# Kernel optimization log

Hardware: AMD Instinct MI355X
Metric: run time of the kernel (lower is better)

## Reference

```python
import jax, jax.numpy as jnp
from jax import lax
import numpy as np

NUM_HEADS = 8
KW = 3  # window kernel size

def _avgpool3(x):
    # x: [B,C,H,W]; AvgPool2d(3,1,1) with count_include_pad=True -> sum/9
    s = lax.reduce_window(x, 0.0, lax.add, (1, 1, KW, KW), (1, 1, 1, 1),
                          ((0, 0), (0, 0), (1, 1), (1, 1)))
    return s / (KW * KW)

def _unfold3(y):
    # y: [B,h,w,C] -> [B,h,w,9,C]; patch index ordered row-major (kh,kw)
    B, h, w, C = y.shape
    yp = jnp.pad(y, ((0, 0), (1, 1), (1, 1), (0, 0)))
    return jnp.stack([yp[:, i:i + h, j:j + w, :]
                      for i in range(KW) for j in range(KW)], axis=3)

def setup_inputs():
    key = jax.random.key(0)
    ks = jax.random.split(key, 9)
    B, C, H, W = 8, 256, 64, 64
    sd = 0.02
    return {
        "x": jax.random.normal(ks[0], (B, C, H, W), jnp.float32),
        "W_qkv": jax.random.normal(ks[1], (4 * C, C), jnp.float32) * sd,
        "b_qkv": jnp.zeros((4 * C,), jnp.float32),
        "W1": jax.random.normal(ks[2], (C // 2, C), jnp.float32) * sd,
        "b1": jnp.zeros((C // 2,), jnp.float32),
        "W2": jax.random.normal(ks[3], (C, C // 2), jnp.float32) * sd,
        "b2": jnp.zeros((C,), jnp.float32),
        "Wp": jax.random.normal(ks[4], (C, C), jnp.float32) * sd,
        "bp": jnp.zeros((C,), jnp.float32),
    }

def reference(x, W_qkv, b_qkv, W1, b1, W2, b2, Wp, bp):
    B, C, H, W = x.shape
    nH = NUM_HEADS
    hd = C // nH
    scale = hd ** -0.5
    # avg pool (stride 1 keeps spatial dims), to channels-last
    y = _avgpool3(x).transpose(0, 2, 3, 1)                 # [B,h,w,C]
    qkv = y @ W_qkv.T + b_qkv                              # [B,h,w,4C]
    qkv = qkv.reshape(B, H, W, C, 4)
    q, k, v, chans = qkv[..., 0], qkv[..., 1], qkv[..., 2], qkv[..., 3]
    # channel gate
    g = jax.nn.sigmoid(jax.nn.relu(chans @ W1.T + b1) @ W2.T + b2)  # [B,h,w,C]
    # local window attention: each query attends to its 3x3 neighborhood
    qh = q.reshape(B, H, W, nH, hd)                        # [B,h,w,n,d]
    kp = _unfold3(k).reshape(B, H, W, KW * KW, nH, hd)     # [B,h,w,9,n,d]
    vp = _unfold3(v).reshape(B, H, W, KW * KW, nH, hd)
    attn = jnp.einsum('bhwnd,bhwknd->bhwnk', qh, kp) * scale
    attn = jax.nn.softmax(attn, axis=-1)
    out = jnp.einsum('bhwnk,bhwknd->bhwnd', attn, vp).reshape(B, H, W, C)
    out = out * g + out
    out = out @ Wp.T + bp
    return out.transpose(0, 3, 1, 2)                       # [B,C,H,W]
```

## Files before the change

### kernel.cpp

```cpp
#include <hip/hip_runtime.h>
#include <stdint.h>

typedef __bf16    bf16x8 __attribute__((ext_vector_type(8)));
typedef float     f32x4  __attribute__((ext_vector_type(4)));
typedef uint32_t  u32x4  __attribute__((ext_vector_type(4)));
typedef uint32_t  u32x2  __attribute__((ext_vector_type(2)));

#define MFMA(a,b,c) __builtin_amdgcn_mfma_f32_16x16x32_bf16((a),(b),(c),0,0,0)

__device__ __align__(16) uint16_t g_y [8*64*64*256];
__device__ __align__(16) uint16_t g_wpk[393216];

#define WQF 0
#define WKF 65536
#define WVF 131072
#define WCF 196608
#define W1F 262144
#define W2F 294912
#define WPF 327680

static __device__ __forceinline__ float b2f(uint32_t u){ return __builtin_bit_cast(float, u<<16); }
static __device__ __forceinline__ float blo(uint32_t u){ return __builtin_bit_cast(float, u<<16); }
static __device__ __forceinline__ float bhi(uint32_t u){ return __builtin_bit_cast(float, u & 0xffff0000u); }
static __device__ __forceinline__ uint16_t f2bn(float f){
  return __builtin_bit_cast(uint16_t, (__bf16)f);
}
static __device__ __forceinline__ uint32_t pk2(float x, float y){
  return (uint32_t)f2bn(x) | ((uint32_t)f2bn(y) << 16);
}

__global__ __launch_bounds__(512) void kprep(const float* __restrict__ x,
    const float* __restrict__ Wqkv, const float* __restrict__ W1,
    const float* __restrict__ W2, const float* __restrict__ Wp){
  int t = threadIdx.x;
  int bid = blockIdx.x;
  if (bid < 1024){
    __shared__ __align__(16) uint16_t sm[3*128*82];
    uint32_t* smw = (uint32_t*)sm;
    int b = bid >> 7, h = (bid >> 1) & 63, ch = (bid & 1) << 7;
    for (int i=t; i<384; i+=512){
      int base = i*41;
      smw[base+3]  = 0;
      smw[base+36] = 0;
    }
    if (h==0 || h==63){
      int hh = (h==0) ? 0 : 2;
      for (int i=t; i<5248; i+=512) smw[hh*5248 + i] = 0;
    }
    #pragma unroll
    for (int i=0;i<12;i++){
      int id = t + 512*i;
      int w4 = id&15, c = (id>>4)&127, hh = id>>11;
      int gy = h - 1 + hh;
      if ((unsigned)gy < 64u){
        f32x4 ld = *(const f32x4*)&x[(((b*256+ch+c)*64+gy)*64) + w4*4];
        int wb = (((hh*128+c)*82 + 8 + w4*4) >> 1);
        smw[wb+0] = pk2(ld[0], ld[1]);
        smw[wb+1] = pk2(ld[2], ld[3]);
      }
    }
    __syncthreads();
    int c = t & 127, wsel = t >> 7;
    int r0 = c*82, r1 = r0 + 128*82, r2 = r1 + 128*82;
    int w0 = wsel*16;
    float csp = b2f(sm[r0+w0+7]) + b2f(sm[r1+w0+7]) + b2f(sm[r2+w0+7]);
    float csc = b2f(sm[r0+w0+8]) + b2f(sm[r1+w0+8]) + b2f(sm[r2+w0+8]);
    uint16_t* dst = g_y + ((b*64+h)*64)*256 + ch + c;
    for (int j2=0;j2<16;j2++){
      int w = w0 + j2;
      float csn = b2f(sm[r0+w+9]) + b2f(sm[r1+w+9]) + b2f(sm[r2+w+9]);
      float yv = (csp + csc + csn) * (1.0f/9.0f);
      dst[w*256] = f2bn(yv);
      csp = csc; csc = csn;
    }
  } else {
    int idx = (bid - 1024)*512 + t;
    int j = idx & 7, lane = (idx>>3)&63;
    int n16 = lane & 15, q4 = lane>>4;
    float v;
    if (idx < 262144){
      int tt = idx >> 16, l = idx & 65535;
      int s = (l>>9)&7, nt = l>>12;
      v = Wqkv[(4*(nt*16+n16) + tt)*256 + s*32 + q4*8 + j];
    } else if (idx < 294912){
      int l = idx - 262144;
      int s = (l>>9)&7, nt = l>>12;
      v = W1[(nt*16+n16)*256 + s*32 + q4*8 + j];
    } else if (idx < 327680){
      int l = idx - 294912;
      int s = (l>>9)&3, nt = l>>11;
      v = W2[(nt*16+n16)*128 + s*32 + q4*8 + j];
    } else {
      int l = idx - 327680;
      int s = (l>>9)&7, nt = l>>12;
      v = Wp[(nt*16+n16)*256 + s*32 + q4*8 + j];
    }
    g_wpk[idx] = f2bn(v);
  }
}

#define YSTR  264
#define QA    15840
#define QB    20192
#define KS    24544
#define VS    32704
#define HSTR  136
#define MCH   0
#define MHS   8448
#define MAO   15840
#define MAOSTR 266
#define MAOT  15840
#define MTSTR 36

static __device__ __forceinline__ void attn_pass(const uint16_t* sm, int qbase,
    int lane, int wave, uint32_t* opk){
  int p = lane & 31, half = lane >> 5;
  int cb = wave*32 + half*16;
  const uint16_t* qp = &sm[qbase + p*HSTR + cb];
  u32x4 qa = *(const u32x4*)qp;
  u32x4 qb = *(const u32x4*)(qp+8);
  float qv[16];
  #pragma unroll
  for (int i=0;i<4;i++){
    qv[2*i]    = blo(qa[i]); qv[2*i+1]   = bhi(qa[i]);
    qv[8+2*i]  = blo(qb[i]); qv[8+2*i+1] = bhi(qb[i]);
  }
  int hb = 10*(p>>3) + (p&7) + 11;
  const int off[9] = {-11,-10,-9,-1,0,1,9,10,11};
  float sc[9];
  #pragma unroll
  for (int nb=0;nb<9;nb++){
    const uint16_t* kp = &sm[KS + (hb+off[nb])*HSTR + cb];
    u32x4 ka = *(const u32x4*)kp;
    u32x4 kb = *(const u32x4*)(kp+8);
    float s = 0.f;
    #pragma unroll
    for (int i=0;i<4;i++){
      s += qv[2*i]*blo(ka[i])   + qv[2*i+1]*bhi(ka[i]);
      s += qv[8+2*i]*blo(kb[i]) + qv[8+2*i+1]*bhi(kb[i]);
    }
    s += __shfl_xor(s, 32);
    sc[nb] = s * 0.17677669529663687f;
  }
  float mx = sc[0];
  #pragma unroll
  for (int nb=1;nb<9;nb++) mx = fmaxf(mx, sc[nb]);
  float l = 0.f;
  #pragma unroll
  for (int nb=0;nb<9;nb++){ sc[nb] = __expf(sc[nb]-mx); l += sc[nb]; }
  float inv = 1.f / l;
  float o[16];
  #pragma unroll
  for (int i=0;i<16;i++) o[i]=0.f;
  #pragma unroll
  for (int nb=0;nb<9;nb++){
    float wgt = sc[nb]*inv;
    const uint16_t* vp = &sm[VS + (hb+off[nb])*HSTR + cb];
    u32x4 va = *(const u32x4*)vp;
    u32x4 vb = *(const u32x4*)(vp+8);
    #pragma unroll
    for (int i=0;i<4;i++){
      o[2*i]    += wgt*blo(va[i]); o[2*i+1]   += wgt*bhi(va[i]);
      o[8+2*i]  += wgt*blo(vb[i]); o[8+2*i+1] += wgt*bhi(vb[i]);
    }
  }
  #pragma unroll
  for (int i=0;i<8;i++) opk[i] = pk2(o[2*i], o[2*i+1]);
}

__global__ __launch_bounds__(512,4) void kattn(const float* __restrict__ bqkv,
    const float* __restrict__ b1, const float* __restrict__ b2v,
    const float* __restrict__ bp, float* __restrict__ out){
  __shared__ __align__(16) uint16_t sm[40864];
  int t = threadIdx.x;
  int lane = t & 63, wave = t >> 6;
  int n16 = lane & 15, quad = lane >> 4;
  int bid = blockIdx.x;
  int bb = bid >> 7, ty = (bid >> 3) & 15, tx = bid & 7;

  uint32_t opk0[8], opk1[8];
  uint32_t chp[8];

  int hrow0 = 10*(n16>>3) + (n16&7) + 11;
  int hrow1 = hrow0 + 20;

  #pragma unroll
  for (int i=0;i<4;i++){
    int id = t + 512*i;
    if (id < 1920){
      int hp = id >> 5, c8 = id & 31;
      int py = hp/10, px = hp - py*10;
      int gy = ty*4 + py - 1, gx = tx*8 + px - 1;
      u32x4 ld = {0,0,0,0};
      if ((unsigned)gy<64u && (unsigned)gx<64u)
        ld = *(const u32x4*)&g_y[((bb*64+gy)*64+gx)*256 + c8*8];
      *(u32x4*)&sm[hp*YSTR + c8*8] = ld;
    }
  }
  __syncthreads();

  {
    int ntgQ = wave, ntC0 = wave*2, ntC1 = wave*2+1;
    f32x4 aq0={0.f,0.f,0.f,0.f}, aq1={0.f,0.f,0.f,0.f};
    f32x4 c00={0.f,0.f,0.f,0.f}, c01={0.f,0.f,0.f,0.f};
    f32x4 c10={0.f,0.f,0.f,0.f}, c11={0.f,0.f,0.f,0.f};
    #pragma unroll
    for (int s=0;s<8;s++){
      bf16x8 Bq  = *(const bf16x8*)&g_wpk[WQF + ((ntgQ*8+s)*64+lane)*8];
      bf16x8 Bc0 = *(const bf16x8*)&g_wpk[WCF + ((ntC0*8+s)*64+lane)*8];
      bf16x8 Bc1 = *(const bf16x8*)&g_wpk[WCF + ((ntC1*8+s)*64+lane)*8];
      bf16x8 A0 = *(const bf16x8*)&sm[hrow0*YSTR + s*32 + quad*8];
      bf16x8 A1 = *(const bf16x8*)&sm[hrow1*YSTR + s*32 + quad*8];
      aq0 = MFMA(A0,Bq,aq0);  aq1 = MFMA(A1,Bq,aq1);
      c00 = MFMA(A0,Bc0,c00); c01 = MFMA(A1,Bc0,c01);
      c10 = MFMA(A0,Bc1,c10); c11 = MFMA(A1,Bc1,c11);
    }
    float bq  = bqkv[4*(ntgQ*16+n16) + 0];
    float bc0 = bqkv[4*(ntC0*16+n16) + 3];
    float bc1 = bqkv[4*(ntC1*16+n16) + 3];
    int colB = wave*16;
    #pragma unroll
    for (int r=0;r<4;r++){
      sm[QA + (quad*4+r)*HSTR + colB + n16]      = f2bn(aq0[r]+bq);
      sm[QA + (16+quad*4+r)*HSTR + colB + n16]   = f2bn(aq1[r]+bq);
    }
    chp[0] = pk2(c00[0]+bc0, c00[1]+bc0); chp[1] = pk2(c00[2]+bc0, c00[3]+bc0);
    chp[2] = pk2(c01[0]+bc0, c01[1]+bc0); chp[3] = pk2(c01[2]+bc0, c01[3]+bc0);
    chp[4] = pk2(c10[0]+bc1, c10[1]+bc1); chp[5] = pk2(c10[2]+bc1, c10[3]+bc1);
    chp[6] = pk2(c11[0]+bc1, c11[1]+bc1); chp[7] = pk2(c11[2]+bc1, c11[3]+bc1);
  }
  {
    int ntg = wave;
    bf16x8 Bk[8], Bv[8];
    #pragma unroll
    for (int s=0;s<8;s++){
      Bk[s] = *(const bf16x8*)&g_wpk[WKF + ((ntg*8+s)*64+lane)*8];
      Bv[s] = *(const bf16x8*)&g_wpk[WVF + ((ntg*8+s)*64+lane)*8];
    }
    float bk = bqkv[4*(ntg*16+n16) + 1];
    float bv = bqkv[4*(ntg*16+n16) + 2];
    int colB = wave*16;
    #pragma unroll
    for (int mt=0; mt<4; mt++){
      f32x4 ak = {0.f,0.f,0.f,0.f}, av = {0.f,0.f,0.f,0.f};
      int m = mt*16 + n16;
      int mr = (m < 60) ? m : 59;
      #pragma unroll
      for (int s=0;s<8;s++){
        bf16x8 A = *(const bf16x8*)&sm[mr*YSTR + s*32 + quad*8];
        ak = MFMA(A, Bk[s], ak);
        av = MFMA(A, Bv[s], av);
      }
      #pragma unroll
      for (int r=0;r<4;r++){
        int row = mt*16 + quad*4 + r;
        if (row < 60){
          int py = row/10, px = row - py*10;
          int gy = ty*4 + py - 1, gx = tx*8 + px - 1;
          bool ok = ((unsigned)gy<64u) && ((unsigned)gx<64u);
          sm[KS + row*HSTR + colB + n16] = ok ? f2bn(ak[r] + bk) : (uint16_t)0;
          sm[VS + row*HSTR + colB + n16] = ok ? f2bn(av[r] + bv) : (uint16_t)0;
        }
      }
    }
  }
  __syncthreads();

  if (wave < 4){
    attn_pass(sm, QA, lane, wave, opk0);
  } else {
    int nt0 = 8 + (wave-4)*2, nt1 = nt0 + 1;
    f32x4 a00={0.f,0.f,0.f,0.f}, a01={0.f,0.f,0.f,0.f};
    f32x4 a10={0.f,0.f,0.f,0.f}, a11={0.f,0.f,0.f,0.f};
    #pragma unroll
    for (int s=0;s<8;s++){
      bf16x8 B0 = *(const bf16x8*)&g_wpk[WQF + ((nt0*8+s)*64+lane)*8];
      bf16x8 B1 = *(const bf16x8*)&g_wpk[WQF + ((nt1*8+s)*64+lane)*8];
      bf16x8 A0 = *(const bf16x8*)&sm[hrow0*YSTR + s*32 + quad*8];
      bf16x8 A1 = *(const bf16x8*)&sm[hrow1*YSTR + s*32 + quad*8];
      a00 = MFMA(A0,B0,a00); a01 = MFMA(A1,B0,a01);
      a10 = MFMA(A0,B1,a10); a11 = MFMA(A1,B1,a11);
    }
    float bq0 = bqkv[4*(nt0*16+n16) + 0];
    float bq1 = bqkv[4*(nt1*16+n16) + 0];
    int c0 = (nt0-8)*16, c1 = (nt1-8)*16;
    #pragma unroll
    for (int r=0;r<4;r++){
      sm[QB + (quad*4+r)*HSTR + c0 + n16]    = f2bn(a00[r]+bq0);
      sm[QB + (16+quad*4+r)*HSTR + c0 + n16] = f2bn(a01[r]+bq0);
      sm[QB + (quad*4+r)*HSTR + c1 + n16]    = f2bn(a10[r]+bq1);
      sm[QB + (16+quad*4+r)*HSTR + c1 + n16] = f2bn(a11[r]+bq1);
    }
  }
  __syncthreads();

  {
    int ntg = 8 + wave;
    bf16x8 Bk[8], Bv[8];
    #pragma unroll
    for (int s=0;s<8;s++){
      Bk[s] = *(const bf16x8*)&g_wpk[WKF + ((ntg*8+s)*64+lane)*8];
      Bv[s] = *(const bf16x8*)&g_wpk[WVF + ((ntg*8+s)*64+lane)*8];
    }
    float bk = bqkv[4*(ntg*16+n16) + 1];
    float bv = bqkv[4*(ntg*16+n16) + 2];
    int colB = wave*16;
    #pragma unroll
    for (int mt=0; mt<4; mt++){
      f32x4 ak = {0.f,0.f,0.f,0.f}, av = {0.f,0.f,0.f,0.f};
      int m = mt*16 + n16;
      int mr = (m < 60) ? m : 59;
      #pragma unroll
      for (int s=0;s<8;s++){
        bf16x8 A = *(const bf16x8*)&sm[mr*YSTR + s*32 + quad*8];
        ak = MFMA(A, Bk[s], ak);
        av = MFMA(A, Bv[s], av);
      }
      #pragma unroll
      for (int r=0;r<4;r++){
        int row = mt*16 + quad*4 + r;
        if (row < 60){
          int py = row/10, px = row - py*10;
          int gy = ty*4 + py - 1, gx = tx*8 + px - 1;
          bool ok = ((unsigned)gy<64u) && ((unsigned)gx<64u);
          sm[KS + row*HSTR + colB + n16] = ok ? f2bn(ak[r] + bk) : (uint16_t)0;
          sm[VS + row*HSTR + colB + n16] = ok ? f2bn(av[r] + bv) : (uint16_t)0;
        }
      }
    }
  }
  __syncthreads();

  #pragma unroll
  for (int jj=0;jj<2;jj++){
    int col = (wave*2+jj)*16 + n16;
    #pragma unroll
    for (int mt=0;mt<2;mt++){
      #pragma unroll
      for (int r2=0;r2<2;r2++){
        uint32_t v = chp[(jj*2+mt)*2+r2];
        int row = mt*16 + quad*4 + r2*2;
        sm[MCH + row*264 + col]     = (uint16_t)(v & 0xffffu);
        sm[MCH + (row+1)*264 + col] = (uint16_t)(v >> 16);
      }
    }
  }
  if (wave < 4) attn_pass(sm, QB, lane, wave, opk1);
  __syncthreads();

  if (wave < 4){
    int p = lane & 31, half = lane >> 5;
    int cb = wave*32 + half*16;
    #pragma unroll
    for (int i=0;i<8;i++){
      *(uint32_t*)&sm[MAO + p*MAOSTR + cb + 2*i]       = opk0[i];
      *(uint32_t*)&sm[MAO + p*MAOSTR + 128 + cb + 2*i] = opk1[i];
    }
  }
  {
    int ntg = wave;
    bf16x8 Bf[8];
    #pragma unroll
    for (int s=0;s<8;s++) Bf[s] = *(const bf16x8*)&g_wpk[W1F + ((ntg*8+s)*64+lane)*8];
    float bs = b1[ntg*16+n16];
    int colB = wave*16;
    #pragma unroll
    for (int mt=0;mt<2;mt++){
      f32x4 a = {0.f,0.f,0.f,0.f};
      #pragma unroll
      for (int s=0;s<8;s++){
        bf16x8 A = *(const bf16x8*)&sm[MCH + (mt*16+n16)*264 + s*32 + quad*8];
        a = MFMA(A, Bf[s], a);
      }
      #pragma unroll
      for (int r=0;r<4;r++){
        int row = mt*16 + quad*4 + r;
        sm[MHS + row*HSTR + colB + n16] = f2bn(fmaxf(a[r]+bs, 0.f));
      }
    }
  }
  __syncthreads();

  {
    int nt0 = wave*2, nt1 = nt0+1;
    f32x4 g00={0.f,0.f,0.f,0.f}, g01={0.f,0.f,0.f,0.f};
    f32x4 g10={0.f,0.f,0.f,0.f}, g11={0.f,0.f,0.f,0.f};
    #pragma unroll
    for (int s=0;s<4;s++){
      bf16x8 B0 = *(const bf16x8*)&g_wpk[W2F + ((nt0*4+s)*64+lane)*8];
      bf16x8 B1 = *(const bf16x8*)&g_wpk[W2F + ((nt1*4+s)*64+lane)*8];
      bf16x8 A0 = *(const bf16x8*)&sm[MHS + n16*HSTR + s*32 + quad*8];
      bf16x8 A1 = *(const bf16x8*)&sm[MHS + (16+n16)*HSTR + s*32 + quad*8];
      g00 = MFMA(A0,B0,g00); g01 = MFMA(A1,B0,g01);
      g10 = MFMA(A0,B1,g10); g11 = MFMA(A1,B1,g11);
    }
    float bs0 = b2v[nt0*16+n16], bs1 = b2v[nt1*16+n16];
    #pragma unroll
    for (int jj=0;jj<2;jj++){
      int colB = (wave*2+jj)*16;
      float bs = jj ? bs1 : bs0;
      #pragma unroll
      for (int mt=0;mt<2;mt++){
        f32x4 a = jj ? (mt ? g11 : g10) : (mt ? g01 : g00);
        #pragma unroll
        for (int r=0;r<4;r++){
          int row = mt*16 + quad*4 + r;
          float gg = 1.f/(1.f+__expf(-(a[r] + bs)));
          float ao = b2f((uint32_t)sm[MAO + row*MAOSTR + colB + n16]);
          sm[MCH + row*264 + colB + n16] = f2bn(ao*(1.f+gg));
        }
      }
    }
  }
  __syncthreads();

  {
    int nt0 = wave*2, nt1 = nt0+1;
    f32x4 p00={0.f,0.f,0.f,0.f}, p01={0.f,0.f,0.f,0.f};
    f32x4 p10={0.f,0.f,0.f,0.f}, p11={0.f,0.f,0.f,0.f};
    #pragma unroll
    for (int s=0;s<8;s++){
      bf16x8 B0 = *(const bf16x8*)&g_wpk[WPF + ((nt0*8+s)*64+lane)*8];
      bf16x8 B1 = *(const bf16x8*)&g_wpk[WPF + ((nt1*8+s)*64+lane)*8];
      bf16x8 A0 = *(const bf16x8*)&sm[MCH + n16*264 + s*32 + quad*8];
      bf16x8 A1 = *(const bf16x8*)&sm[MCH + (16+n16)*264 + s*32 + quad*8];
      p00 = MFMA(A0,B0,p00); p01 = MFMA(A1,B0,p01);
      p10 = MFMA(A0,B1,p10); p11 = MFMA(A1,B1,p11);
    }
    float bs0 = bp[nt0*16+n16], bs1 = bp[nt1*16+n16];
    #pragma unroll
    for (int jj=0;jj<2;jj++){
      int col = (wave*2+jj)*16 + n16;
      float bs = jj ? bs1 : bs0;
      #pragma unroll
      for (int mt=0;mt<2;mt++){
        f32x4 a = jj ? (mt ? p11 : p10) : (mt ? p01 : p00);
        u32x2 pk = { pk2(a[0]+bs, a[1]+bs), pk2(a[2]+bs, a[3]+bs) };
        int row0 = mt*16 + quad*4;
        *(u32x2*)&sm[MAOT + col*MTSTR + row0] = pk;
      }
    }
  }
  __syncthreads();

  #pragma unroll
  for (int i=0;i<4;i++){
    int idx = t + 512*i;
    int ix4 = idx&1, iy = (idx>>1)&3, c = idx>>3;
    int p0 = iy*8 + ix4*4;
    u32x2 pk = *(const u32x2*)&sm[MAOT + c*MTSTR + p0];
    f32x4 stv;
    stv[0] = blo(pk[0]); stv[1] = bhi(pk[0]);
    stv[2] = blo(pk[1]); stv[3] = bhi(pk[1]);
    *(f32x4*)&out[(((bb*256+c)*64) + ty*4+iy)*64 + tx*8 + ix4*4] = stv;
  }
}

extern "C" void kernel_launch(void* const* d_in, const int* in_sizes, int n_in,
                              void* d_out, int out_size, void* d_ws, size_t ws_size,
                              hipStream_t stream){
  (void)in_sizes; (void)n_in; (void)d_ws; (void)ws_size; (void)out_size;
  const float* x    = (const float*)d_in[0];
  const float* Wqkv = (const float*)d_in[1];
  const float* bqkv = (const float*)d_in[2];
  const float* W1   = (const float*)d_in[3];
  const float* b1   = (const float*)d_in[4];
  const float* W2   = (const float*)d_in[5];
  const float* b2   = (const float*)d_in[6];
  const float* Wp   = (const float*)d_in[7];
  const float* bp   = (const float*)d_in[8];
  kprep<<<dim3(1792), dim3(512), 0, stream>>>(x, Wqkv, W1, W2, Wp);
  kattn<<<dim3(1024), dim3(512), 0, stream>>>(bqkv, b1, b2, bp, (float*)d_out);
}
```

Measured before the change: 188.5 us.

## Move channel-gate GEMM to idle attention-phase waves and restructure GEMM loops

The channel-projection GEMM is taken out of the first phase and given to waves 4-7, which run it while waves 0-3 do the first attention pass. Each of these waves now computes four channel tiles and holds sixteen packed registers until it writes them to shared memory during the second attention pass. The K/V GEMM is factored into a helper, and the Q GEMM and the W2/Wp GEMMs are reorganised to loop over tiles with per-tile weight registers. This moves work into the phase where half the block was idle, at the cost of an extra barrier, more register pressure in waves 4-7, and less interleaving of independent MFMAs.

```diff
diff --git a/kernel.cpp b/kernel.cpp
--- a/kernel.cpp
+++ b/kernel.cpp
@@ -168,6 +168,42 @@
   for (int i=0;i<8;i++) opk[i] = pk2(o[2*i], o[2*i+1]);
 }
 
+static __device__ __forceinline__ void kv_gemm(uint16_t* sm, int ntg,
+    const float* bqkv, int lane, int wave, int n16, int quad, int ty, int tx){
+  bf16x8 Bk[8], Bv[8];
+  #pragma unroll
+  for (int s=0;s<8;s++){
+    Bk[s] = *(const bf16x8*)&g_wpk[WKF + ((ntg*8+s)*64+lane)*8];
+    Bv[s] = *(const bf16x8*)&g_wpk[WVF + ((ntg*8+s)*64+lane)*8];
+  }
+  float bk = bqkv[4*(ntg*16+n16) + 1];
+  float bv = bqkv[4*(ntg*16+n16) + 2];
+  int colB = wave*16;
+  #pragma unroll
+  for (int mt=0; mt<4; mt++){
+    f32x4 ak = {0.f,0.f,0.f,0.f}, av = {0.f,0.f,0.f,0.f};
+    int m = mt*16 + n16;
+    int mr = (m < 60) ? m : 59;
+    #pragma unroll
+    for (int s=0;s<8;s++){
+      bf16x8 A = *(const bf16x8*)&sm[mr*YSTR + s*32 + quad*8];
+      ak = MFMA(A, Bk[s], ak);
+      av = MFMA(A, Bv[s], av);
+    }
+    #pragma unroll
+    for (int r=0;r<4;r++){
+      int row = mt*16 + quad*4 + r;
+      if (row < 60){
+        int py = row/10, px = row - py*10;
+        int gy = ty*4 + py - 1, gx = tx*8 + px - 1;
+        bool ok = ((unsigned)gy<64u) && ((unsigned)gx<64u);
+        sm[KS + row*HSTR + colB + n16] = ok ? f2bn(ak[r] + bk) : (uint16_t)0;
+        sm[VS + row*HSTR + colB + n16] = ok ? f2bn(av[r] + bv) : (uint16_t)0;
+      }
+    }
+  }
+}
+
 __global__ __launch_bounds__(512,4) void kattn(const float* __restrict__ bqkv,
     const float* __restrict__ b1, const float* __restrict__ b2v,
     const float* __restrict__ bp, float* __restrict__ out){
@@ -179,7 +215,7 @@
   int bb = bid >> 7, ty = (bid >> 3) & 15, tx = bid & 7;
 
   uint32_t opk0[8], opk1[8];
-  uint32_t chp[8];
+  uint32_t chp[16];
 
   int hrow0 = 10*(n16>>3) + (n16&7) + 11;
   int hrow1 = hrow0 + 20;
@@ -200,75 +236,59 @@
   __syncthreads();
 
   {
-    int ntgQ = wave, ntC0 = wave*2, ntC1 = wave*2+1;
-    f32x4 aq0={0.f,0.f,0.f,0.f}, aq1={0.f,0.f,0.f,0.f};
-    f32x4 c00={0.f,0.f,0.f,0.f}, c01={0.f,0.f,0.f,0.f};
-    f32x4 c10={0.f,0.f,0.f,0.f}, c11={0.f,0.f,0.f,0.f};
-    #pragma unroll
-    for (int s=0;s<8;s++){
-      bf16x8 Bq  = *(const bf16x8*)&g_wpk[WQF + ((ntgQ*8+s)*64+lane)*8];
-      bf16x8 Bc0 = *(const bf16x8*)&g_wpk[WCF + ((ntC0*8+s)*64+lane)*8];
-      bf16x8 Bc1 = *(const bf16x8*)&g_wpk[WCF + ((ntC1*8+s)*64+lane)*8];
-      bf16x8 A0 = *(const bf16x8*)&sm[hrow0*YSTR + s*32 + quad*8];
-      bf16x8 A1 = *(const bf16x8*)&sm[hrow1*YSTR + s*32 + quad*8];
-      aq0 = MFMA(A0,Bq,aq0);  aq1 = MFMA(A1,Bq,aq1);
-      c00 = MFMA(A0,Bc0,c00); c01 = MFMA(A1,Bc0,c01);
-      c10 = MFMA(A0,Bc1,c10); c11 = MFMA(A1,Bc1,c11);
-    }
-    float bq  = bqkv[4*(ntgQ*16+n16) + 0];
-    float bc0 = bqkv[4*(ntC0*16+n16) + 3];
-    float bc1 = bqkv[4*(ntC1*16+n16) + 3];
+    int ntg = wave;
+    bf16x8 Bq[8];
+    #pragma unroll
+    for (int s=0;s<8;s++) Bq[s] = *(const bf16x8*)&g_wpk[WQF + ((ntg*8+s)*64+lane)*8];
+    float bq = bqkv[4*(ntg*16+n16) + 0];
     int colB = wave*16;
     #pragma unroll
-    for (int r=0;r<4;r++){
-      sm[QA + (quad*4+r)*HSTR + colB + n16]      = f2bn(aq0[r]+bq);
-      sm[QA + (16+quad*4+r)*HSTR + colB + n16]   = f2bn(aq1[r]+bq);
-    }
-    chp[0] = pk2(c00[0]+bc0, c00[1]+bc0); chp[1] = pk2(c00[2]+bc0, c00[3]+bc0);
-    chp[2] = pk2(c01[0]+bc0, c01[1]+bc0); chp[3] = pk2(c01[2]+bc0, c01[3]+bc0);
-    chp[4] = pk2(c10[0]+bc1, c10[1]+bc1); chp[5] = pk2(c10[2]+bc1, c10[3]+bc1);
-    chp[6] = pk2(c11[0]+bc1, c11[1]+bc1); chp[7] = pk2(c11[2]+bc1, c11[3]+bc1);
-  }
-  {
-    int ntg = wave;
-    bf16x8 Bk[8], Bv[8];
-    #pragma unroll
-    for (int s=0;s<8;s++){
-      Bk[s] = *(const bf16x8*)&g_wpk[WKF + ((ntg*8+s)*64+lane)*8];
-      Bv[s] = *(const bf16x8*)&g_wpk[WVF + ((ntg*8+s)*64+lane)*8];
-    }
-    float bk = bqkv[4*(ntg*16+n16) + 1];
-    float bv = bqkv[4*(ntg*16+n16) + 2];
-    int colB = wave*16;
-    #pragma unroll
-    for (int mt=0; mt<4; mt++){
-      f32x4 ak = {0.f,0.f,0.f,0.f}, av = {0.f,0.f,0.f,0.f};
-      int m = mt*16 + n16;
-      int mr = (m < 60) ? m : 59;
+    for (int mt=0; mt<2; mt++){
+      f32x4 a = {0.f,0.f,0.f,0.f};
+      int hrow = mt ? hrow1 : hrow0;
       #pragma unroll
       for (int s=0;s<8;s++){
-        bf16x8 A = *(const bf16x8*)&sm[mr*YSTR + s*32 + quad*8];
-        ak = MFMA(A, Bk[s], ak);
-        av = MFMA(A, Bv[s], av);
-      }
-      #pragma unroll
-      for (int r=0;r<4;r++){
-        int row = mt*16 + quad*4 + r;
-        if (row < 60){
-          int py = row/10, px = row - py*10;
-          int gy = ty*4 + py - 1, gx = tx*8 + px - 1;
-          bool ok = ((unsigned)gy<64u) && ((unsigned)gx<64u);
-          sm[KS + row*HSTR + colB + n16] = ok ? f2bn(ak[r] + bk) : (uint16_t)0;
-          sm[VS + row*HSTR + colB + n16] = ok ? f2bn(av[r] + bv) : (uint16_t)0;
-        }
-      }
-    }
-  }
+        bf16x8 A = *(const bf16x8*)&sm[hrow*YSTR + s*32 + quad*8];
+        a = MFMA(A, Bq[s], a);
+      }
+      #pragma unroll
+      for (int r=0;r<4;r++)
+        sm[QA + (mt*16 + quad*4 + r)*HSTR + colB + n16] = f2bn(a[r] + bq);
+    }
+  }
+  __syncthreads();
+
+  kv_gemm(sm, wave, bqkv, lane, wave, n16, quad, ty, tx);
   __syncthreads();
 
   if (wave < 4){
     attn_pass(sm, QA, lane, wave, opk0);
   } else {
+    f32x4 cc[4][2];
+    #pragma unroll
+    for (int jj=0;jj<4;jj++){ cc[jj][0] = f32x4{0.f,0.f,0.f,0.f}; cc[jj][1] = f32x4{0.f,0.f,0.f,0.f}; }
+    #pragma unroll
+    for (int s=0;s<8;s++){
+      bf16x8 A0 = *(const bf16x8*)&sm[hrow0*YSTR + s*32 + quad*8];
+      bf16x8 A1 = *(const bf16x8*)&sm[hrow1*YSTR + s*32 + quad*8];
+      #pragma unroll
+      for (int jj=0;jj<4;jj++){
+        int ntg = (wave-4)*4 + jj;
+        bf16x8 Bc = *(const bf16x8*)&g_wpk[WCF + ((ntg*8+s)*64+lane)*8];
+        cc[jj][0] = MFMA(A0, Bc, cc[jj][0]);
+        cc[jj][1] = MFMA(A1, Bc, cc[jj][1]);
+      }
+    }
+    #pragma unroll
+    for (int jj=0;jj<4;jj++){
+      int ntg = (wave-4)*4 + jj;
+      float bc = bqkv[4*(ntg*16+n16) + 3];
+      #pragma unroll
+      for (int mt=0;mt<2;mt++){
+        chp[(jj*2+mt)*2+0] = pk2(cc[jj][mt][0]+bc, cc[jj][mt][1]+bc);
+        chp[(jj*2+mt)*2+1] = pk2(cc[jj][mt][2]+bc, cc[jj][mt][3]+bc);
+      }
+    }
     int nt0 = 8 + (wave-4)*2, nt1 = nt0 + 1;
     f32x4 a00={0.f,0.f,0.f,0.f}, a01={0.f,0.f,0.f,0.f};
     f32x4 a10={0.f,0.f,0.f,0.f}, a11={0.f,0.f,0.f,0.f};
@@ -294,58 +314,28 @@
   }
   __syncthreads();
 
-  {
-    int ntg = 8 + wave;
-    bf16x8 Bk[8], Bv[8];
-    #pragma unroll
-    for (int s=0;s<8;s++){
-      Bk[s] = *(const bf16x8*)&g_wpk[WKF + ((ntg*8+s)*64+lane)*8];
-      Bv[s] = *(const bf16x8*)&g_wpk[WVF + ((ntg*8+s)*64+lane)*8];
-    }
-    float bk = bqkv[4*(ntg*16+n16) + 1];
-    float bv = bqkv[4*(ntg*16+n16) + 2];
-    int colB = wave*16;
-    #pragma unroll
-    for (int mt=0; mt<4; mt++){
-      f32x4 ak = {0.f,0.f,0.f,0.f}, av = {0.f,0.f,0.f,0.f};
-      int m = mt*16 + n16;
-      int mr = (m < 60) ? m : 59;
-      #pragma unroll
-      for (int s=0;s<8;s++){
-        bf16x8 A = *(const bf16x8*)&sm[mr*YSTR + s*32 + quad*8];
-        ak = MFMA(A, Bk[s], ak);
-        av = MFMA(A, Bv[s], av);
-      }
-      #pragma unroll
-      for (int r=0;r<4;r++){
-        int row = mt*16 + quad*4 + r;
-        if (row < 60){
-          int py = row/10, px = row - py*10;
-          int gy = ty*4 + py - 1, gx = tx*8 + px - 1;
-          bool ok = ((unsigned)gy<64u) && ((unsigned)gx<64u);
-          sm[KS + row*HSTR + colB + n16] = ok ? f2bn(ak[r] + bk) : (uint16_t)0;
-          sm[VS + row*HSTR + colB + n16] = ok ? f2bn(av[r] + bv) : (uint16_t)0;
+  kv_gemm(sm, 8 + wave, bqkv, lane, wave, n16, quad, ty, tx);
+  __syncthreads();
+
+  if (wave < 4){
+    attn_pass(sm, QB, lane, wave, opk1);
+  } else {
+    #pragma unroll
+    for (int jj=0;jj<4;jj++){
+      int ntg = (wave-4)*4 + jj;
+      int col = ntg*16 + n16;
+      #pragma unroll
+      for (int mt=0;mt<2;mt++){
+        #pragma unroll
+        for (int r2=0;r2<2;r2++){
+          uint32_t v = chp[(jj*2+mt)*2+r2];
+          int row = mt*16 + quad*4 + r2*2;
+          sm[MCH + row*264 + col]     = (uint16_t)(v & 0xffffu);
+          sm[MCH + (row+1)*264 + col] = (uint16_t)(v >> 16);
         }
       }
     }
   }
-  __syncthreads();
-
-  #pragma unroll
-  for (int jj=0;jj<2;jj++){
-    int col = (wave*2+jj)*16 + n16;
-    #pragma unroll
-    for (int mt=0;mt<2;mt++){
-      #pragma unroll
-      for (int r2=0;r2<2;r2++){
-        uint32_t v = chp[(jj*2+mt)*2+r2];
-        int row = mt*16 + quad*4 + r2*2;
-        sm[MCH + row*264 + col]     = (uint16_t)(v & 0xffffu);
-        sm[MCH + (row+1)*264 + col] = (uint16_t)(v >> 16);
-      }
-    }
-  }
-  if (wave < 4) attn_pass(sm, QB, lane, wave, opk1);
   __syncthreads();
 
   if (wave < 4){
@@ -381,64 +371,52 @@
   }
   __syncthreads();
 
-  {
-    int nt0 = wave*2, nt1 = nt0+1;
-    f32x4 g00={0.f,0.f,0.f,0.f}, g01={0.f,0.f,0.f,0.f};
-    f32x4 g10={0.f,0.f,0.f,0.f}, g11={0.f,0.f,0.f,0.f};
-    #pragma unroll
-    for (int s=0;s<4;s++){
-      bf16x8 B0 = *(const bf16x8*)&g_wpk[W2F + ((nt0*4+s)*64+lane)*8];
-      bf16x8 B1 = *(const bf16x8*)&g_wpk[W2F + ((nt1*4+s)*64+lane)*8];
-      bf16x8 A0 = *(const bf16x8*)&sm[MHS + n16*HSTR + s*32 + quad*8];
-      bf16x8 A1 = *(const bf16x8*)&sm[MHS + (16+n16)*HSTR + s*32 + quad*8];
-      g00 = MFMA(A0,B0,g00); g01 = MFMA(A1,B0,g01);
-      g10 = MFMA(A0,B1,g10); g11 = MFMA(A1,B1,g11);
-    }
-    float bs0 = b2v[nt0*16+n16], bs1 = b2v[nt1*16+n16];
-    #pragma unroll
-    for (int jj=0;jj<2;jj++){
-      int colB = (wave*2+jj)*16;
-      float bs = jj ? bs1 : bs0;
-      #pragma unroll
-      for (int mt=0;mt<2;mt++){
-        f32x4 a = jj ? (mt ? g11 : g10) : (mt ? g01 : g00);
-        #pragma unroll
-        for (int r=0;r<4;r++){
-          int row = mt*16 + quad*4 + r;
-          float gg = 1.f/(1.f+__expf(-(a[r] + bs)));
-          float ao = b2f((uint32_t)sm[MAO + row*MAOSTR + colB + n16]);
-          sm[MCH + row*264 + colB + n16] = f2bn(ao*(1.f+gg));
-        }
-      }
-    }
-  }
-  __syncthreads();
-
-  {
-    int nt0 = wave*2, nt1 = nt0+1;
-    f32x4 p00={0.f,0.f,0.f,0.f}, p01={0.f,0.f,0.f,0.f};
-    f32x4 p10={0.f,0.f,0.f,0.f}, p11={0.f,0.f,0.f,0.f};
-    #pragma unroll
-    for (int s=0;s<8;s++){
-      bf16x8 B0 = *(const bf16x8*)&g_wpk[WPF + ((nt0*8+s)*64+lane)*8];
-      bf16x8 B1 = *(const bf16x8*)&g_wpk[WPF + ((nt1*8+s)*64+lane)*8];
-      bf16x8 A0 = *(const bf16x8*)&sm[MCH + n16*264 + s*32 + quad*8];
-      bf16x8 A1 = *(const bf16x8*)&sm[MCH + (16+n16)*264 + s*32 + quad*8];
-      p00 = MFMA(A0,B0,p00); p01 = MFMA(A1,B0,p01);
-      p10 = MFMA(A0,B1,p10); p11 = MFMA(A1,B1,p11);
-    }
-    float bs0 = bp[nt0*16+n16], bs1 = bp[nt1*16+n16];
-    #pragma unroll
-    for (int jj=0;jj<2;jj++){
-      int col = (wave*2+jj)*16 + n16;
-      float bs = jj ? bs1 : bs0;
-      #pragma unroll
-      for (int mt=0;mt<2;mt++){
-        f32x4 a = jj ? (mt ? p11 : p10) : (mt ? p01 : p00);
-        u32x2 pk = { pk2(a[0]+bs, a[1]+bs), pk2(a[2]+bs, a[3]+bs) };
-        int row0 = mt*16 + quad*4;
-        *(u32x2*)&sm[MAOT + col*MTSTR + row0] = pk;
-      }
+  #pragma unroll
+  for (int jj=0;jj<2;jj++){
+    int ntg = wave*2 + jj;
+    bf16x8 Bf[4];
+    #pragma unroll
+    for (int s=0;s<4;s++) Bf[s] = *(const bf16x8*)&g_wpk[W2F + ((ntg*4+s)*64+lane)*8];
+    float bs = b2v[ntg*16+n16];
+    int colB = ntg*16;
+    #pragma unroll
+    for (int mt=0;mt<2;mt++){
+      f32x4 a = {0.f,0.f,0.f,0.f};
+      #pragma unroll
+      for (int s=0;s<4;s++){
+        bf16x8 A = *(const bf16x8*)&sm[MHS + (mt*16+n16)*HSTR + s*32 + quad*8];
+        a = MFMA(A, Bf[s], a);
+      }
+      #pragma unroll
+      for (int r=0;r<4;r++){
+        int row = mt*16 + quad*4 + r;
+        float gg = 1.f/(1.f+__expf(-(a[r] + bs)));
+        float ao = b2f((uint32_t)sm[MAO + row*MAOSTR + colB + n16]);
+        sm[MCH + row*264 + colB + n16] = f2bn(ao*(1.f+gg));
+      }
+    }
+  }
+  __syncthreads();
+
+  #pragma unroll
+  for (int jj=0;jj<2;jj++){
+    int ntg = wave*2 + jj;
+    bf16x8 Bf[8];
+    #pragma unroll
+    for (int s=0;s<8;s++) Bf[s] = *(const bf16x8*)&g_wpk[WPF + ((ntg*8+s)*64+lane)*8];
+    float bs = bp[ntg*16+n16];
+    int colB = ntg*16;
+    #pragma unroll
+    for (int mt=0;mt<2;mt++){
+      f32x4 a = {0.f,0.f,0.f,0.f};
+      #pragma unroll
+      for (int s=0;s<8;s++){
+        bf16x8 A = *(const bf16x8*)&sm[MCH + (mt*16+n16)*264 + s*32 + quad*8];
+        a = MFMA(A, Bf[s], a);
+      }
+      u32x2 pk = { pk2(a[0]+bs, a[1]+bs), pk2(a[2]+bs, a[3]+bs) };
+      int col = colB + n16, row0 = mt*16 + quad*4;
+      *(u32x2*)&sm[MAOT + col*MTSTR + row0] = pk;
     }
   }
   __syncthreads();
```

Result: slower. 193.5 us (+2.6%).
